# Kernel optimization log

Hardware: AMD Instinct MI355X
Metric: run time of the kernel (lower is better)

Reference implementation:

```python
import jax, jax.numpy as jnp
import numpy as np

S = 1024          # tokens (prefill)
DIM = 2560
HEAD_DIM = 128
N_HEADS = 20
N_KV = 5
HPG = N_HEADS // N_KV      # heads per kv group = 4
GS = 128                   # weight-scale group size
THETA = 500000.0
EPS = 1e-05
QKV_OUT = (N_HEADS + 2 * N_KV) * HEAD_DIM  # 3840


def setup_inputs() -> dict:
    key = jax.random.key(0)
    ks = jax.random.split(key, 7)
    x = jax.random.normal(ks[0], (S, DIM), jnp.float32)
    # unpacked int2 (ternary) weights, stored as float for the reference math
    w_qkv = jax.random.randint(ks[1], (QKV_OUT, DIM), -1, 2).astype(jnp.float32)
    ws_qkv = jax.random.uniform(ks[2], (QKV_OUT, DIM // GS), jnp.float32, 0.01, 0.05)
    w_o = jax.random.randint(ks[3], (DIM, N_HEADS * HEAD_DIM), -1, 2).astype(jnp.float32)
    ws_o = jax.random.uniform(ks[4], (DIM, N_HEADS * HEAD_DIM // GS), jnp.float32, 0.01, 0.05)
    q_norm_w = 1.0 + 0.02 * jax.random.normal(ks[5], (HEAD_DIM,), jnp.float32)
    k_norm_w = 1.0 + 0.02 * jax.random.normal(ks[6], (HEAD_DIM,), jnp.float32)
    return {"x": x, "w_qkv": w_qkv, "ws_qkv": ws_qkv, "w_o": w_o, "ws_o": ws_o,
            "q_norm_w": q_norm_w, "k_norm_w": k_norm_w}


def _quant_act(x):
    # per-token symmetric int8 quant: s = 127 / max|x| (clamped)
    s = 127.0 / jnp.clip(jnp.max(jnp.abs(x), axis=-1, keepdims=True), 1e-05, None)
    q = jnp.clip(jnp.round(x * s), -128.0, 127.0)
    return q, s


def _bitlinear(x, w, ws):
    # int8 activation x int2 weight GEMM with per-(out,group) dequant scales
    q, s = _quant_act(x)
    w_dq = w * jnp.repeat(ws, GS, axis=1)        # [out, in]
    return (q @ w_dq.T) / s


def _rmsnorm(x, w):
    return x * jax.lax.rsqrt(jnp.mean(x * x, axis=-1, keepdims=True) + EPS) * w


def _rope(x, cos, sin):
    # x: [S, ..., d]; cos/sin: [S, d//2], interleaved-pair (llama) convention
    d2 = x.shape[-1] // 2
    shape = (x.shape[0],) + (1,) * (x.ndim - 2) + (d2,)
    c = cos.reshape(shape)
    s = sin.reshape(shape)
    xr = x.reshape(x.shape[:-1] + (d2, 2))
    x0, x1 = xr[..., 0], xr[..., 1]
    out = jnp.stack([x0 * c - x1 * s, x0 * s + x1 * c], axis=-1)
    return out.reshape(x.shape)


def reference(x, w_qkv, ws_qkv, w_o, ws_o, q_norm_w, k_norm_w):
    qkv = _bitlinear(x, w_qkv, ws_qkv)                       # [S, 3840]
    q_size = N_HEADS * HEAD_DIM
    k_size = N_KV * HEAD_DIM
    xq = qkv[:, :q_size].reshape(S, N_KV, HPG, HEAD_DIM)     # [S, g, h, d]
    xk = qkv[:, q_size:q_size + k_size].reshape(S, N_KV, HEAD_DIM)
    xv = qkv[:, q_size + k_size:].reshape(S, N_KV, HEAD_DIM)
    xq = _rmsnorm(xq, q_norm_w)
    xk = _rmsnorm(xk, k_norm_w)
    # RoPE (prefill: positions 0..S-1)
    pos = jnp.arange(S, dtype=jnp.float32)
    inv_freq = THETA ** (-jnp.arange(0, HEAD_DIM, 2, dtype=jnp.float32) / HEAD_DIM)
    ang = pos[:, None] * inv_freq[None, :]                   # [S, d/2]
    cos, sin = jnp.cos(ang), jnp.sin(ang)
    xq = _rope(xq, cos, sin)
    xk = _rope(xk, cos, sin)
    # GQA causal flash-attention math
    scale = HEAD_DIM ** -0.5
    scores = jnp.einsum('sghd,tgd->ghst', xq, xk) * scale    # [g, h, S, S]
    causal = jnp.tril(jnp.ones((S, S), bool))
    scores = jnp.where(causal, scores, -1e30)
    attn = jax.nn.softmax(scores, axis=-1)
    out = jnp.einsum('ghst,tgd->sghd', attn, xv).reshape(S, N_HEADS * HEAD_DIM)
    return _bitlinear(out, w_o, ws_o)                        # [S, DIM]
```

## Files before the change

kernel.cpp:

```cpp
#include <hip/hip_runtime.h>
#include <hip/hip_bf16.h>
#include <cstdint>
#include <math.h>

#define SEQ 1024
#define DIM 2560
#define HD 128
#define NH 20
#define NKV 5
#define QKV_OUT 3840
#define GS 128

typedef __bf16 bf16;
typedef __bf16 bf16x4 __attribute__((ext_vector_type(4)));
typedef __bf16 bf16x8 __attribute__((ext_vector_type(8)));
typedef float f32x4 __attribute__((ext_vector_type(4)));

__global__ __launch_bounds__(256) void quant_kernel(
    const float* __restrict__ x, bf16* __restrict__ act,
    float* __restrict__ rs, int cols) {
  const int row = blockIdx.x;
  const int tid = threadIdx.x;
  const float* xr = x + (size_t)row * cols;
  float m = 0.f;
  for (int i = tid; i < cols; i += 256) m = fmaxf(m, fabsf(xr[i]));
  for (int off = 32; off; off >>= 1) m = fmaxf(m, __shfl_xor(m, off));
  __shared__ float red[4];
  __shared__ float s_bc;
  if ((tid & 63) == 0) red[tid >> 6] = m;
  __syncthreads();
  if (tid == 0) {
    float mm = fmaxf(fmaxf(red[0], red[1]), fmaxf(red[2], red[3]));
    mm = fmaxf(mm, 1e-5f);
    s_bc = 127.f / mm;
    rs[row] = mm / 127.f;
  }
  __syncthreads();
  const float s = s_bc;
  bf16* ar = act + (size_t)row * cols;
  for (int i = tid; i < cols; i += 256) {
    float q = rintf(xr[i] * s);
    q = fminf(fmaxf(q, -128.f), 127.f);
    ar[i] = (bf16)q;
  }
}

__global__ __launch_bounds__(256) void dequant_kernel(
    const float* __restrict__ w, const float* __restrict__ ws,
    bf16* __restrict__ wdq, int K, long total4) {
  long i = (long)blockIdx.x * 256 + threadIdx.x;
  if (i >= total4) return;
  long e = i * 4;
  int row = (int)(e / K);
  int k = (int)(e % K);
  float sc = ws[(size_t)row * (K / GS) + (k / GS)];
  float4 wv = *(const float4*)(w + e);
  bf16x4 o;
  o[0] = (bf16)(wv.x * sc);
  o[1] = (bf16)(wv.y * sc);
  o[2] = (bf16)(wv.z * sc);
  o[3] = (bf16)(wv.w * sc);
  *(bf16x4*)(wdq + e) = o;
}

__device__ __forceinline__ void gload_lds16(const bf16* g, bf16* l) {
  __builtin_amdgcn_global_load_lds(
      (const __attribute__((address_space(1))) void*)g,
      (__attribute__((address_space(3))) void*)l, 16, 0, 0);
}

template <int OUT_BF16>
__global__ __launch_bounds__(256) void gemm_bt(
    const bf16* __restrict__ A, const bf16* __restrict__ B,
    const float* __restrict__ rs, void* __restrict__ C, int N, int K) {
  __shared__ bf16 As[64 * 64];
  __shared__ bf16 Bs[128 * 64];
  const int tid = threadIdx.x;
  const int w = tid >> 6, l = tid & 63;
  const int row0 = blockIdx.y * 64;
  const int col0 = blockIdx.x * 128;
  const int wm = (w >> 1) * 32, wn = (w & 1) * 64;
  const int lcol = l & 15, quad = l >> 4;
  const int sr = l >> 3;
  const int sk = (l & 7) * 8;
  const bf16* Ag = A + (size_t)row0 * K;
  const bf16* Bg = B + (size_t)col0 * K;

  f32x4 acc[2][4] = {};

  for (int k0 = 0; k0 < K; k0 += 64) {
    __syncthreads();
#pragma unroll
    for (int i = 0; i < 2; ++i) {
      int rb = w * 16 + i * 8;
      gload_lds16(Ag + (size_t)(rb + sr) * K + k0 + sk, As + rb * 64);
    }
#pragma unroll
    for (int i = 0; i < 4; ++i) {
      int rb = w * 32 + i * 8;
      gload_lds16(Bg + (size_t)(rb + sr) * K + k0 + sk, Bs + rb * 64);
    }
    __syncthreads();
#pragma unroll
    for (int ks = 0; ks < 2; ++ks) {
      const int kk = ks * 32 + quad * 8;
      bf16x8 af[2], bff[4];
#pragma unroll
      for (int mi = 0; mi < 2; ++mi)
        af[mi] = *(const bf16x8*)(As + (wm + mi * 16 + lcol) * 64 + kk);
#pragma unroll
      for (int ni = 0; ni < 4; ++ni)
        bff[ni] = *(const bf16x8*)(Bs + (wn + ni * 16 + lcol) * 64 + kk);
#pragma unroll
      for (int mi = 0; mi < 2; ++mi)
#pragma unroll
        for (int ni = 0; ni < 4; ++ni)
          acc[mi][ni] = __builtin_amdgcn_mfma_f32_16x16x32_bf16(
              af[mi], bff[ni], acc[mi][ni], 0, 0, 0);
    }
  }
#pragma unroll
  for (int mi = 0; mi < 2; ++mi) {
#pragma unroll
    for (int ni = 0; ni < 4; ++ni) {
      int col = col0 + wn + ni * 16 + lcol;
#pragma unroll
      for (int r = 0; r < 4; ++r) {
        int row = row0 + wm + mi * 16 + quad * 4 + r;
        float v = acc[mi][ni][r] * rs[row];
        if (OUT_BF16)
          ((bf16*)C)[(size_t)row * N + col] = (bf16)v;
        else
          ((float*)C)[(size_t)row * N + col] = v;
      }
    }
  }
}

__global__ void qk_post(const float* __restrict__ qkv,
                        const float* __restrict__ qw, const float* __restrict__ kw,
                        bf16* __restrict__ Qo, bf16* __restrict__ Ko) {
  const int t = blockIdx.x, h = blockIdx.y, i = threadIdx.x;
  const float* src = (h < NH)
      ? qkv + (size_t)t * QKV_OUT + h * HD
      : qkv + (size_t)t * QKV_OUT + 2560 + (h - NH) * HD;
  float x0 = src[2 * i], x1 = src[2 * i + 1];
  float ss = x0 * x0 + x1 * x1;
  for (int off = 1; off < 64; off <<= 1) ss += __shfl_xor(ss, off);
  float r = rsqrtf(ss * (1.f / 128.f) + 1e-5f);
  const float* wv = (h < NH) ? qw : kw;
  float y0 = x0 * r * wv[2 * i];
  float y1 = x1 * r * wv[2 * i + 1];
  float inv_freq = powf(500000.f, -(float)(2 * i) * (1.f / 128.f));
  float ang = (float)t * inv_freq;
  float sn, cs;
  sincosf(ang, &sn, &cs);
  float o0 = y0 * cs - y1 * sn;
  float o1 = y0 * sn + y1 * cs;
  if (h < NH) {
    bf16* dst = Qo + ((size_t)t * NH + h) * HD + 2 * i;
    dst[0] = (bf16)o0; dst[1] = (bf16)o1;
  } else {
    bf16* dst = Ko + ((size_t)(h - NH) * SEQ + t) * HD + 2 * i;
    dst[0] = (bf16)o0; dst[1] = (bf16)o1;
  }
}

__global__ __launch_bounds__(256) void v_post(const float* __restrict__ qkv,
                                              bf16* __restrict__ Vt) {
  const int t0 = blockIdx.x * 64, g = blockIdx.y;
  const int tid = threadIdx.x;
  __shared__ bf16 Ls[64 * 137];
  {
    const int tl = tid >> 4;
    const int d0 = (tid & 15) * 8;
#pragma unroll
    for (int pass = 0; pass < 4; ++pass) {
      int t = pass * 16 + tl;
      const float* src = qkv + (size_t)(t0 + t) * QKV_OUT + 3200 + g * HD + d0;
      float4 a = *(const float4*)src;
      float4 b = *(const float4*)(src + 4);
      bf16* dst = Ls + t * 137 + d0;
      dst[0] = (bf16)a.x; dst[1] = (bf16)a.y; dst[2] = (bf16)a.z; dst[3] = (bf16)a.w;
      dst[4] = (bf16)b.x; dst[5] = (bf16)b.y; dst[6] = (bf16)b.z; dst[7] = (bf16)b.w;
    }
  }
  __syncthreads();
  {
    const int dl = tid >> 3;
    const int tl0 = (tid & 7) * 8;
#pragma unroll
    for (int pass = 0; pass < 4; ++pass) {
      int d = pass * 32 + dl;
      bf16x8 v;
#pragma unroll
      for (int j = 0; j < 8; ++j) v[j] = Ls[(tl0 + j) * 137 + d];
      *(bf16x8*)(Vt + ((size_t)g * HD + d) * SEQ + t0 + tl0) = v;
    }
  }
}

__global__ __launch_bounds__(128) void attn_mfma(
    const bf16* __restrict__ Qb, const bf16* __restrict__ Kb,
    const bf16* __restrict__ Vt, float* __restrict__ O) {
  const int qb = 31 - (int)blockIdx.x;
  const int H = blockIdx.y, g = H >> 2;
  const int tid = threadIdx.x;
  const int wave = tid >> 6, lane = tid & 63;
  const int qcol = lane & 15, quad = lane >> 4;
  const int q_tok = qb * 32 + wave * 16 + qcol;
  const float scale = 0.08838834764831843f;

  __shared__ bf16 Ks[64 * 128];
  __shared__ bf16 Vs[128 * 64];

  const bf16* kbase = Kb + (size_t)g * SEQ * HD;
  const bf16* vbase = Vt + (size_t)g * HD * SEQ;

  bf16x8 qf[4];
  {
    const bf16* qp = Qb + ((size_t)q_tok * NH + H) * HD + quad * 8;
#pragma unroll
    for (int kc = 0; kc < 4; ++kc) qf[kc] = *(const bf16x8*)(qp + kc * 32);
  }

  float m_i = -1e30f, l_i = 0.f;
  f32x4 o_acc[8] = {};
  const int kt_max = (qb * 32 + 31) >> 6;

  const int k_r = lane >> 4, k_g = lane & 15;
  const int v_r = lane >> 3, v_g = lane & 7;

  for (int kt = 0; kt <= kt_max; ++kt) {
    const int key0 = kt * 64;
    __syncthreads();
#pragma unroll
    for (int p = 0; p < 8; ++p) {
      int r0 = (wave * 8 + p) * 4;
      int r = r0 + k_r;
      gload_lds16(kbase + (size_t)(key0 + r) * HD + ((k_g ^ (r & 15)) * 8),
                  Ks + r0 * 128);
    }
#pragma unroll
    for (int p = 0; p < 8; ++p) {
      int r0 = (wave * 8 + p) * 8;
      int r = r0 + v_r;
      gload_lds16(vbase + (size_t)r * SEQ + key0 + ((v_g ^ (r & 7)) * 8),
                  Vs + r0 * 64);
    }
    __syncthreads();

    f32x4 s[4];
#pragma unroll
    for (int mg = 0; mg < 4; ++mg) {
      const int R = mg * 16 + qcol;
      const bf16* krow = Ks + R * 128;
      f32x4 acc = {0.f, 0.f, 0.f, 0.f};
#pragma unroll
      for (int kc = 0; kc < 4; ++kc) {
        int j = kc * 4 + quad;
        bf16x8 kf = *(const bf16x8*)(krow + ((j ^ (R & 15)) * 8));
        acc = __builtin_amdgcn_mfma_f32_16x16x32_bf16(kf, qf[kc], acc, 0, 0, 0);
      }
      s[mg] = acc;
    }

    float mt = -1e30f;
#pragma unroll
    for (int mg = 0; mg < 4; ++mg)
#pragma unroll
      for (int r = 0; r < 4; ++r) {
        int key = key0 + mg * 16 + quad * 4 + r;
        float v = (key <= q_tok) ? s[mg][r] * scale : -1e30f;
        s[mg][r] = v;
        mt = fmaxf(mt, v);
      }
    mt = fmaxf(mt, __shfl_xor(mt, 16));
    mt = fmaxf(mt, __shfl_xor(mt, 32));
    float mnew = fmaxf(m_i, mt);
    float alpha = __expf(m_i - mnew);
    float ps = 0.f;
#pragma unroll
    for (int mg = 0; mg < 4; ++mg)
#pragma unroll
      for (int r = 0; r < 4; ++r) {
        float pv = __expf(s[mg][r] - mnew);
        s[mg][r] = pv;
        ps += pv;
      }
    ps += __shfl_xor(ps, 16);
    ps += __shfl_xor(ps, 32);
    l_i = l_i * alpha + ps;
    m_i = mnew;
#pragma unroll
    for (int mg2 = 0; mg2 < 8; ++mg2)
#pragma unroll
      for (int r = 0; r < 4; ++r) o_acc[mg2][r] *= alpha;

    bf16x8 pb[2];
#pragma unroll
    for (int c = 0; c < 2; ++c)
#pragma unroll
      for (int j = 0; j < 8; ++j)
        pb[c][j] = (bf16)s[c * 2 + (j >> 2)][j & 3];

#pragma unroll
    for (int mg2 = 0; mg2 < 8; ++mg2) {
      const int R = mg2 * 16 + qcol;
      const bf16* vrow = Vs + R * 64;
      f32x4 acc = o_acc[mg2];
#pragma unroll
      for (int c = 0; c < 2; ++c) {
        int g8a = c * 8 + quad;
        int g8b = c * 8 + 4 + quad;
        bf16x4 v0 = *(const bf16x4*)(vrow + ((g8a >> 1) ^ (R & 7)) * 8 + (g8a & 1) * 4);
        bf16x4 v1 = *(const bf16x4*)(vrow + ((g8b >> 1) ^ (R & 7)) * 8 + (g8b & 1) * 4);
        bf16x8 vfr;
#pragma unroll
        for (int j = 0; j < 4; ++j) { vfr[j] = v0[j]; vfr[j + 4] = v1[j]; }
        acc = __builtin_amdgcn_mfma_f32_16x16x32_bf16(vfr, pb[c], acc, 0, 0, 0);
      }
      o_acc[mg2] = acc;
    }
  }

  const float inv = 1.f / l_i;
  float* op = O + (size_t)q_tok * DIM + H * HD + quad * 4;
#pragma unroll
  for (int mg2 = 0; mg2 < 8; ++mg2) {
    float4 vv = make_float4(o_acc[mg2][0] * inv, o_acc[mg2][1] * inv,
                            o_acc[mg2][2] * inv, o_acc[mg2][3] * inv);
    *(float4*)(op + mg2 * 16) = vv;
  }
}

extern "C" void kernel_launch(void* const* d_in, const int* in_sizes, int n_in,
                              void* d_out, int out_size, void* d_ws, size_t ws_size,
                              hipStream_t stream) {
  const float* x      = (const float*)d_in[0];
  const float* w_qkv  = (const float*)d_in[1];
  const float* ws_qkv = (const float*)d_in[2];
  const float* w_o    = (const float*)d_in[3];
  const float* ws_o   = (const float*)d_in[4];
  const float* qnw    = (const float*)d_in[5];
  const float* knw    = (const float*)d_in[6];
  float* out = (float*)d_out;

  char* p = (char*)d_ws;
  bf16*  act1 = (bf16*)p;  p += (size_t)SEQ * DIM * 2;
  float* rs1  = (float*)p; p += 4096;
  bf16*  wqdq = (bf16*)p;  p += (size_t)QKV_OUT * DIM * 2;
  bf16*  wodq = (bf16*)p;  p += (size_t)DIM * DIM * 2;
  float* qkv  = (float*)p; p += (size_t)SEQ * QKV_OUT * 4;
  bf16*  Qb   = (bf16*)p;  p += (size_t)SEQ * NH * HD * 2;
  bf16*  Kb   = (bf16*)p;  p += (size_t)NKV * SEQ * HD * 2;
  bf16*  Vt   = (bf16*)p;  p += (size_t)NKV * HD * SEQ * 2;
  float* attn = (float*)p; p += (size_t)SEQ * DIM * 4;
  bf16*  act2 = (bf16*)p;  p += (size_t)SEQ * DIM * 2;
  float* rs2  = (float*)p; p += 4096;

  quant_kernel<<<SEQ, 256, 0, stream>>>(x, act1, rs1, DIM);
  {
    long t4 = (long)QKV_OUT * DIM / 4;
    dequant_kernel<<<(int)((t4 + 255) / 256), 256, 0, stream>>>(w_qkv, ws_qkv, wqdq, DIM, t4);
  }
  {
    long t4 = (long)DIM * DIM / 4;
    dequant_kernel<<<(int)((t4 + 255) / 256), 256, 0, stream>>>(w_o, ws_o, wodq, DIM, t4);
  }
  gemm_bt<0><<<dim3(QKV_OUT / 128, SEQ / 64), 256, 0, stream>>>(act1, wqdq, rs1, qkv, QKV_OUT, DIM);
  qk_post<<<dim3(SEQ, 25), 64, 0, stream>>>(qkv, qnw, knw, Qb, Kb);
  v_post<<<dim3(SEQ / 64, NKV), 256, 0, stream>>>(qkv, Vt);
  attn_mfma<<<dim3(32, NH), 128, 0, stream>>>(Qb, Kb, Vt, attn);
  quant_kernel<<<SEQ, 256, 0, stream>>>(attn, act2, rs2, DIM);
  gemm_bt<0><<<dim3(DIM / 128, SEQ / 64), 256, 0, stream>>>(act2, wodq, rs2, out, DIM, DIM);
}
```

Measured before the change: 272.1 us.

## Split-K both GEMMs into two halves and XOR-swizzle LDS tiles

Both bitlinear GEMMs now split the K dimension in two across blockIdx.z, each half writing a separate fp32 partial buffer. The QKV partials are summed inside qk_post and v_post, and the output partials by a new add2 kernel. This doubles the block count so more CUs are busy on the small grids (30x16 and 20x16). LDS tiles are also XOR-swizzled by row to reduce bank conflicts on the fragment reads. The cost is extra fp32 partial-buffer traffic plus one extra kernel launch.

```diff
diff --git a/kernel.cpp b/kernel.cpp
--- a/kernel.cpp
+++ b/kernel.cpp
@@ -69,48 +69,54 @@
       (__attribute__((address_space(3))) void*)l, 16, 0, 0);
 }
 
-template <int OUT_BF16>
 __global__ __launch_bounds__(256) void gemm_bt(
     const bf16* __restrict__ A, const bf16* __restrict__ B,
-    const float* __restrict__ rs, void* __restrict__ C, int N, int K) {
+    const float* __restrict__ rs, float* __restrict__ C,
+    int N, int K, int Kh, size_t part_stride) {
   __shared__ bf16 As[64 * 64];
   __shared__ bf16 Bs[128 * 64];
   const int tid = threadIdx.x;
   const int w = tid >> 6, l = tid & 63;
   const int row0 = blockIdx.y * 64;
   const int col0 = blockIdx.x * 128;
+  const int z = blockIdx.z;
   const int wm = (w >> 1) * 32, wn = (w & 1) * 64;
   const int lcol = l & 15, quad = l >> 4;
   const int sr = l >> 3;
-  const int sk = (l & 7) * 8;
-  const bf16* Ag = A + (size_t)row0 * K;
-  const bf16* Bg = B + (size_t)col0 * K;
+  const int sg = l & 7;
+  const bf16* Ag = A + (size_t)row0 * K + (size_t)z * Kh;
+  const bf16* Bg = B + (size_t)col0 * K + (size_t)z * Kh;
 
   f32x4 acc[2][4] = {};
 
-  for (int k0 = 0; k0 < K; k0 += 64) {
+  for (int k0 = 0; k0 < Kh; k0 += 64) {
     __syncthreads();
 #pragma unroll
     for (int i = 0; i < 2; ++i) {
       int rb = w * 16 + i * 8;
-      gload_lds16(Ag + (size_t)(rb + sr) * K + k0 + sk, As + rb * 64);
+      int r = rb + sr;
+      gload_lds16(Ag + (size_t)r * K + k0 + ((sg ^ (r & 7)) * 8), As + rb * 64);
     }
 #pragma unroll
     for (int i = 0; i < 4; ++i) {
       int rb = w * 32 + i * 8;
-      gload_lds16(Bg + (size_t)(rb + sr) * K + k0 + sk, Bs + rb * 64);
+      int r = rb + sr;
+      gload_lds16(Bg + (size_t)r * K + k0 + ((sg ^ (r & 7)) * 8), Bs + rb * 64);
     }
     __syncthreads();
 #pragma unroll
     for (int ks = 0; ks < 2; ++ks) {
-      const int kk = ks * 32 + quad * 8;
       bf16x8 af[2], bff[4];
 #pragma unroll
-      for (int mi = 0; mi < 2; ++mi)
-        af[mi] = *(const bf16x8*)(As + (wm + mi * 16 + lcol) * 64 + kk);
-#pragma unroll
-      for (int ni = 0; ni < 4; ++ni)
-        bff[ni] = *(const bf16x8*)(Bs + (wn + ni * 16 + lcol) * 64 + kk);
+      for (int mi = 0; mi < 2; ++mi) {
+        int R = wm + mi * 16 + lcol;
+        af[mi] = *(const bf16x8*)(As + R * 64 + (((ks * 4 + quad) ^ (R & 7)) * 8));
+      }
+#pragma unroll
+      for (int ni = 0; ni < 4; ++ni) {
+        int R = wn + ni * 16 + lcol;
+        bff[ni] = *(const bf16x8*)(Bs + R * 64 + (((ks * 4 + quad) ^ (R & 7)) * 8));
+      }
 #pragma unroll
       for (int mi = 0; mi < 2; ++mi)
 #pragma unroll
@@ -119,6 +125,7 @@
               af[mi], bff[ni], acc[mi][ni], 0, 0, 0);
     }
   }
+  float* Cp = C + (size_t)z * part_stride;
 #pragma unroll
   for (int mi = 0; mi < 2; ++mi) {
 #pragma unroll
@@ -127,26 +134,35 @@
 #pragma unroll
       for (int r = 0; r < 4; ++r) {
         int row = row0 + wm + mi * 16 + quad * 4 + r;
-        float v = acc[mi][ni][r] * rs[row];
-        if (OUT_BF16)
-          ((bf16*)C)[(size_t)row * N + col] = (bf16)v;
-        else
-          ((float*)C)[(size_t)row * N + col] = v;
-      }
-    }
-  }
-}
-
-__global__ void qk_post(const float* __restrict__ qkv,
+        Cp[(size_t)row * N + col] = acc[mi][ni][r] * rs[row];
+      }
+    }
+  }
+}
+
+__global__ __launch_bounds__(256) void add2_kernel(
+    const float* __restrict__ a, const float* __restrict__ b,
+    float* __restrict__ o, int n4) {
+  int i = blockIdx.x * 256 + threadIdx.x;
+  if (i >= n4) return;
+  float4 x = ((const float4*)a)[i];
+  float4 y = ((const float4*)b)[i];
+  ((float4*)o)[i] = make_float4(x.x + y.x, x.y + y.y, x.z + y.z, x.w + y.w);
+}
+
+__global__ void qk_post(const float* __restrict__ qkvA, const float* __restrict__ qkvB,
                         const float* __restrict__ qw, const float* __restrict__ kw,
                         bf16* __restrict__ Qo, bf16* __restrict__ Ko) {
   const int t = blockIdx.x, h = blockIdx.y, i = threadIdx.x;
-  const float* src = (h < NH)
-      ? qkv + (size_t)t * QKV_OUT + h * HD
-      : qkv + (size_t)t * QKV_OUT + 2560 + (h - NH) * HD;
-  float x0 = src[2 * i], x1 = src[2 * i + 1];
+  const size_t off = (h < NH)
+      ? (size_t)t * QKV_OUT + h * HD
+      : (size_t)t * QKV_OUT + 2560 + (h - NH) * HD;
+  const float* s1 = qkvA + off;
+  const float* s2 = qkvB + off;
+  float x0 = s1[2 * i] + s2[2 * i];
+  float x1 = s1[2 * i + 1] + s2[2 * i + 1];
   float ss = x0 * x0 + x1 * x1;
-  for (int off = 1; off < 64; off <<= 1) ss += __shfl_xor(ss, off);
+  for (int off2 = 1; off2 < 64; off2 <<= 1) ss += __shfl_xor(ss, off2);
   float r = rsqrtf(ss * (1.f / 128.f) + 1e-5f);
   const float* wv = (h < NH) ? qw : kw;
   float y0 = x0 * r * wv[2 * i];
@@ -166,7 +182,8 @@
   }
 }
 
-__global__ __launch_bounds__(256) void v_post(const float* __restrict__ qkv,
+__global__ __launch_bounds__(256) void v_post(const float* __restrict__ qkvA,
+                                              const float* __restrict__ qkvB,
                                               bf16* __restrict__ Vt) {
   const int t0 = blockIdx.x * 64, g = blockIdx.y;
   const int tid = threadIdx.x;
@@ -177,12 +194,16 @@
 #pragma unroll
     for (int pass = 0; pass < 4; ++pass) {
       int t = pass * 16 + tl;
-      const float* src = qkv + (size_t)(t0 + t) * QKV_OUT + 3200 + g * HD + d0;
-      float4 a = *(const float4*)src;
-      float4 b = *(const float4*)(src + 4);
+      size_t off = (size_t)(t0 + t) * QKV_OUT + 3200 + g * HD + d0;
+      float4 a = *(const float4*)(qkvA + off);
+      float4 b = *(const float4*)(qkvA + off + 4);
+      float4 a2 = *(const float4*)(qkvB + off);
+      float4 b2 = *(const float4*)(qkvB + off + 4);
       bf16* dst = Ls + t * 137 + d0;
-      dst[0] = (bf16)a.x; dst[1] = (bf16)a.y; dst[2] = (bf16)a.z; dst[3] = (bf16)a.w;
-      dst[4] = (bf16)b.x; dst[5] = (bf16)b.y; dst[6] = (bf16)b.z; dst[7] = (bf16)b.w;
+      dst[0] = (bf16)(a.x + a2.x); dst[1] = (bf16)(a.y + a2.y);
+      dst[2] = (bf16)(a.z + a2.z); dst[3] = (bf16)(a.w + a2.w);
+      dst[4] = (bf16)(b.x + b2.x); dst[5] = (bf16)(b.y + b2.y);
+      dst[6] = (bf16)(b.z + b2.z); dst[7] = (bf16)(b.w + b2.w);
     }
   }
   __syncthreads();
@@ -351,7 +372,8 @@
   float* rs1  = (float*)p; p += 4096;
   bf16*  wqdq = (bf16*)p;  p += (size_t)QKV_OUT * DIM * 2;
   bf16*  wodq = (bf16*)p;  p += (size_t)DIM * DIM * 2;
-  float* qkv  = (float*)p; p += (size_t)SEQ * QKV_OUT * 4;
+  float* qkvA = (float*)p; p += (size_t)SEQ * QKV_OUT * 4;
+  float* qkvB = (float*)p; p += (size_t)SEQ * QKV_OUT * 4;
   bf16*  Qb   = (bf16*)p;  p += (size_t)SEQ * NH * HD * 2;
   bf16*  Kb   = (bf16*)p;  p += (size_t)NKV * SEQ * HD * 2;
   bf16*  Vt   = (bf16*)p;  p += (size_t)NKV * HD * SEQ * 2;
@@ -359,6 +381,9 @@
   bf16*  act2 = (bf16*)p;  p += (size_t)SEQ * DIM * 2;
   float* rs2  = (float*)p; p += 4096;
 
+  float* outA = qkvA;
+  float* outB = qkvA + (size_t)SEQ * DIM;
+
   quant_kernel<<<SEQ, 256, 0, stream>>>(x, act1, rs1, DIM);
   {
     long t4 = (long)QKV_OUT * DIM / 4;
@@ -368,10 +393,16 @@
     long t4 = (long)DIM * DIM / 4;
     dequant_kernel<<<(int)((t4 + 255) / 256), 256, 0, stream>>>(w_o, ws_o, wodq, DIM, t4);
   }
-  gemm_bt<0><<<dim3(QKV_OUT / 128, SEQ / 64), 256, 0, stream>>>(act1, wqdq, rs1, qkv, QKV_OUT, DIM);
-  qk_post<<<dim3(SEQ, 25), 64, 0, stream>>>(qkv, qnw, knw, Qb, Kb);
-  v_post<<<dim3(SEQ / 64, NKV), 256, 0, stream>>>(qkv, Vt);
+  gemm_bt<<<dim3(QKV_OUT / 128, SEQ / 64, 2), 256, 0, stream>>>(
+      act1, wqdq, rs1, qkvA, QKV_OUT, DIM, DIM / 2, (size_t)SEQ * QKV_OUT);
+  qk_post<<<dim3(SEQ, 25), 64, 0, stream>>>(qkvA, qkvB, qnw, knw, Qb, Kb);
+  v_post<<<dim3(SEQ / 64, NKV), 256, 0, stream>>>(qkvA, qkvB, Vt);
   attn_mfma<<<dim3(32, NH), 128, 0, stream>>>(Qb, Kb, Vt, attn);
   quant_kernel<<<SEQ, 256, 0, stream>>>(attn, act2, rs2, DIM);
-  gemm_bt<0><<<dim3(DIM / 128, SEQ / 64), 256, 0, stream>>>(act2, wodq, rs2, out, DIM, DIM);
-}
+  gemm_bt<<<dim3(DIM / 128, SEQ / 64, 2), 256, 0, stream>>>(
+      act2, wodq, rs2, outA, DIM, DIM, DIM / 2, (size_t)SEQ * DIM);
+  {
+    int n4 = SEQ * DIM / 4;
+    add2_kernel<<<(n4 + 255) / 256, 256, 0, stream>>>(outA, outB, out, n4);
+  }
+}
```

Result: faster. 246.6 us (-9.4%).
